# Kernel optimization log

Hardware: AMD Instinct MI355X
Metric: run time of the kernel (lower is better)

## Reference

```python
import jax, jax.numpy as jnp
import numpy as np

N_NODES = 100000
E = 500000
H = 128  # hidden_channels


def setup_inputs() -> dict:
    key = jax.random.key(0)
    ks = jax.random.split(key, 9)
    return {
        "z_pnode": jax.random.normal(ks[0], (N_NODES, H), dtype=jnp.float32),
        "z_onode": jax.random.normal(ks[1], (N_NODES, H), dtype=jnp.float32),
        "ptnp_edge_label_index": jax.random.randint(ks[2], (2, E), 0, N_NODES, dtype=jnp.int64) if jax.config.jax_enable_x64 else jax.random.randint(ks[2], (2, E), 0, N_NODES, dtype=jnp.int32),
        "nptp_edge_label_index": jax.random.randint(ks[3], (2, E), 0, N_NODES, dtype=jnp.int32),
        "nptnp_edge_label_index": jax.random.randint(ks[4], (2, E), 0, N_NODES, dtype=jnp.int32),
        "w1": jax.random.normal(ks[5], (2 * H, H), dtype=jnp.float32) * (1.0 / np.sqrt(2 * H)),
        "b1": jnp.zeros((H,), dtype=jnp.float32),
        "w2": jax.random.normal(ks[6], (H, 1), dtype=jnp.float32) * (1.0 / np.sqrt(H)),
        "b2": jnp.zeros((1,), dtype=jnp.float32),
    }


def reference(z_pnode, z_onode, ptnp_edge_label_index, nptp_edge_label_index,
              nptnp_edge_label_index, w1, b1, w2, b2):
    # Gather endpoint embeddings per edge type and concat along feature dim.
    z_ptnp = jnp.concatenate(
        [z_pnode[ptnp_edge_label_index[0]], z_onode[ptnp_edge_label_index[1]]], axis=-1)
    z_nptp = jnp.concatenate(
        [z_onode[nptp_edge_label_index[0]], z_pnode[nptp_edge_label_index[1]]], axis=-1)
    z_nptnp = jnp.concatenate(
        [z_onode[nptnp_edge_label_index[0]], z_onode[nptnp_edge_label_index[1]]], axis=-1)
    z = jnp.concatenate([z_ptnp, z_nptp, z_nptnp], axis=0)  # [3E, 2H]
    h = jax.nn.relu(z @ w1 + b1)                             # [3E, H]
    out = h @ w2 + b2                                        # [3E, 1]
    return out.reshape(-1)
```

## Files before the change

### kernel.cpp

```cpp
#include <hip/hip_runtime.h>
#include <hip/hip_bf16.h>
#include <stdint.h>

#define H 128
#define NNODES 100000
#define NEDGE 500000
#define MT 32
#define TILES_PER_Z 3125
#define GEMM_GRID 1024

#define BSW_BYTES 65536
#define TBL_ELEMS (NNODES * H)
#define WS_NEEDED ((size_t)BSW_BYTES + 4ULL * TBL_ELEMS * 2ULL)

typedef __bf16 bf16x8 __attribute__((ext_vector_type(8)));
typedef float f32x4 __attribute__((ext_vector_type(4)));

union frag_cast { uint4 u; bf16x8 b; ushort s[8]; };

__device__ __forceinline__ ushort f2bf(float f) {
    __hip_bfloat16 h = __float2bfloat16(f);
    return *(ushort*)&h;
}

__device__ __forceinline__ void bf2_to_f(uint32_t u, float& lo, float& hi) {
    union { uint32_t i; float f; } a, b;
    a.i = u << 16;
    b.i = u & 0xffff0000u;
    lo = a.f;
    hi = b.f;
}

__global__ __launch_bounds__(256) void prep_bsw(const float* __restrict__ w1,
                                                ushort* __restrict__ bsw) {
    int i = blockIdx.x * 256 + threadIdx.x;
    int j = i & 7;
    int n = (i >> 3) & 255;
    int kb = i >> 11;
    int k = kb * 8 + j;
    int r = (n < 128) ? k : (128 + k);
    int c = n & 127;
    bsw[i] = f2bf(w1[r * H + c]);
}

__global__ __launch_bounds__(256, 3) void gemm_tables(
    const float* __restrict__ zp, const float* __restrict__ zo,
    const ushort* __restrict__ bsw, const float* __restrict__ b1,
    ushort* __restrict__ t_ps, ushort* __restrict__ t_pd,
    ushort* __restrict__ t_os, ushort* __restrict__ t_od) {
    __shared__ float abuf[MT * H];

    const int t = threadIdx.x;
    const int wave = t >> 6;
    const int lane = t & 63;
    const int l15 = lane & 15;
    const int quad = lane >> 4;
    const int n0 = wave * 64;
    const int half = wave >> 1;
    const int colbase = n0 - half * 128;

    frag_cast bfr[4][4];
#pragma unroll
    for (int s = 0; s < 4; ++s)
#pragma unroll
        for (int nt = 0; nt < 4; ++nt)
            bfr[s][nt].u = *(const uint4*)(bsw + ((s * 4 + quad) * 256 + n0 + nt * 16 + l15) * 8);

    float bias[4] = {0.f, 0.f, 0.f, 0.f};
    if (half) {
#pragma unroll
        for (int nt = 0; nt < 4; ++nt)
            bias[nt] = b1[colbase + nt * 16 + l15];
    }

    int src_off[4];
    int lds_off[4];
#pragma unroll
    for (int i = 0; i < 4; ++i) {
        const int r = (wave * 4 + i) * 2 + (lane >> 5);
        const int jsrc = (lane & 31) ^ (r & 15);
        src_off[i] = r * H + jsrc * 4;
        lds_off[i] = (wave * 4 + i) * 256;
    }

    for (int tile = blockIdx.x; tile < 2 * TILES_PER_Z; tile += gridDim.x) {
        const int zsel = tile & 1;
        const int node0 = (tile >> 1) * MT;
        const float* __restrict__ ztile =
            (zsel ? zo : zp) + (size_t)node0 * H;

#pragma unroll
        for (int i = 0; i < 4; ++i) {
            const float* gp = ztile + src_off[i];
            float* lp = abuf + lds_off[i];
            __builtin_amdgcn_global_load_lds(
                (const __attribute__((address_space(1))) uint32_t*)gp,
                (__attribute__((address_space(3))) uint32_t*)lp, 16, 0, 0);
        }
        __syncthreads();

        f32x4 acc[2][4];
#pragma unroll
        for (int mt = 0; mt < 2; ++mt)
#pragma unroll
            for (int nt = 0; nt < 4; ++nt)
                acc[mt][nt] = (f32x4){0.f, 0.f, 0.f, 0.f};

#pragma unroll
        for (int s = 0; s < 4; ++s)
#pragma unroll
            for (int mt = 0; mt < 2; ++mt) {
                const int row = mt * 16 + l15;
                const int c = s * 4 + quad;
                const float4 vlo = *(const float4*)(abuf + row * H + ((2 * c) ^ l15) * 4);
                const float4 vhi = *(const float4*)(abuf + row * H + ((2 * c + 1) ^ l15) * 4);
                frag_cast a;
                a.s[0] = f2bf(vlo.x); a.s[1] = f2bf(vlo.y);
                a.s[2] = f2bf(vlo.z); a.s[3] = f2bf(vlo.w);
                a.s[4] = f2bf(vhi.x); a.s[5] = f2bf(vhi.y);
                a.s[6] = f2bf(vhi.z); a.s[7] = f2bf(vhi.w);
#pragma unroll
                for (int nt = 0; nt < 4; ++nt)
                    acc[mt][nt] = __builtin_amdgcn_mfma_f32_16x16x32_bf16(
                        a.b, bfr[s][nt].b, acc[mt][nt], 0, 0, 0);
            }
        __syncthreads();

        ushort* __restrict__ dst =
            zsel ? (half ? t_od : t_os) : (half ? t_pd : t_ps);
#pragma unroll
        for (int mt = 0; mt < 2; ++mt)
#pragma unroll
            for (int nt = 0; nt < 4; ++nt) {
                const int col = colbase + nt * 16 + l15;
#pragma unroll
                for (int r = 0; r < 4; ++r) {
                    const int grow = node0 + mt * 16 + quad * 4 + r;
                    dst[(size_t)grow * H + col] = f2bf(acc[mt][nt][r] + bias[nt]);
                }
            }
    }
}

__global__ __launch_bounds__(256) void edge_kernel(
    const __hip_bfloat16* __restrict__ t_ps, const __hip_bfloat16* __restrict__ t_pd,
    const __hip_bfloat16* __restrict__ t_os, const __hip_bfloat16* __restrict__ t_od,
    const int* __restrict__ ptnp, const int* __restrict__ nptp,
    const int* __restrict__ nptnp,
    const float* __restrict__ w2, const float* __restrict__ b2,
    float* __restrict__ out) {
    const int tid = blockIdx.x * 256 + threadIdx.x;
    const int g = tid >> 4;
    const int lane = tid & 15;

    const __hip_bfloat16 *src_tbl, *dst_tbl;
    int si, di;
    if (g < NEDGE) {
        si = ptnp[g]; di = ptnp[NEDGE + g];
        src_tbl = t_ps; dst_tbl = t_od;
    } else if (g < 2 * NEDGE) {
        const int e = g - NEDGE;
        si = nptp[e]; di = nptp[NEDGE + e];
        src_tbl = t_os; dst_tbl = t_pd;
    } else {
        const int e = g - 2 * NEDGE;
        si = nptnp[e]; di = nptnp[NEDGE + e];
        src_tbl = t_os; dst_tbl = t_od;
    }

    const uint4 s4 = *(const uint4*)(src_tbl + si * H + lane * 8);
    const uint4 d4 = *(const uint4*)(dst_tbl + di * H + lane * 8);
    const float4 w2a = *(const float4*)(w2 + lane * 8);
    const float4 w2b = *(const float4*)(w2 + lane * 8 + 4);

    float s0, s1, d0, d1;
    float sum = 0.f;
    bf2_to_f(s4.x, s0, s1); bf2_to_f(d4.x, d0, d1);
    sum = fmaf(fmaxf(s0 + d0, 0.f), w2a.x, sum);
    sum = fmaf(fmaxf(s1 + d1, 0.f), w2a.y, sum);
    bf2_to_f(s4.y, s0, s1); bf2_to_f(d4.y, d0, d1);
    sum = fmaf(fmaxf(s0 + d0, 0.f), w2a.z, sum);
    sum = fmaf(fmaxf(s1 + d1, 0.f), w2a.w, sum);
    bf2_to_f(s4.z, s0, s1); bf2_to_f(d4.z, d0, d1);
    sum = fmaf(fmaxf(s0 + d0, 0.f), w2b.x, sum);
    sum = fmaf(fmaxf(s1 + d1, 0.f), w2b.y, sum);
    bf2_to_f(s4.w, s0, s1); bf2_to_f(d4.w, d0, d1);
    sum = fmaf(fmaxf(s0 + d0, 0.f), w2b.z, sum);
    sum = fmaf(fmaxf(s1 + d1, 0.f), w2b.w, sum);

    sum += __shfl_down(sum, 8, 16);
    sum += __shfl_down(sum, 4, 16);
    sum += __shfl_down(sum, 2, 16);
    sum += __shfl_down(sum, 1, 16);
    if (lane == 0) out[g] = sum + b2[0];
}

__global__ __launch_bounds__(128) void edge_direct(
    const float* __restrict__ zp, const float* __restrict__ zo,
    const int* __restrict__ ptnp, const int* __restrict__ nptp,
    const int* __restrict__ nptnp,
    const float* __restrict__ w1, const float* __restrict__ b1,
    const float* __restrict__ w2, const float* __restrict__ b2,
    float* __restrict__ out) {
    const int g = blockIdx.x;
    const int j = threadIdx.x;

    const float *src, *dst;
    int si, di;
    if (g < NEDGE) {
        si = ptnp[g]; di = ptnp[NEDGE + g]; src = zp; dst = zo;
    } else if (g < 2 * NEDGE) {
        const int e = g - NEDGE;
        si = nptp[e]; di = nptp[NEDGE + e]; src = zo; dst = zp;
    } else {
        const int e = g - 2 * NEDGE;
        si = nptnp[e]; di = nptnp[NEDGE + e]; src = zo; dst = zo;
    }
    const float* zs = src + si * H;
    const float* zd = dst + di * H;

    float acc = b1[j];
    for (int k = 0; k < H; ++k) acc = fmaf(zs[k], w1[k * H + j], acc);
    for (int k = 0; k < H; ++k) acc = fmaf(zd[k], w1[(H + k) * H + j], acc);
    float v = fmaxf(acc, 0.f) * w2[j];

    for (int off = 32; off > 0; off >>= 1) v += __shfl_down(v, off, 64);
    __shared__ float parts[2];
    if ((j & 63) == 0) parts[j >> 6] = v;
    __syncthreads();
    if (j == 0) out[g] = parts[0] + parts[1] + b2[0];
}

extern "C" void kernel_launch(void* const* d_in, const int* in_sizes, int n_in,
                              void* d_out, int out_size, void* d_ws, size_t ws_size,
                              hipStream_t stream) {
    const float* zp    = (const float*)d_in[0];
    const float* zo    = (const float*)d_in[1];
    const int*   ptnp  = (const int*)d_in[2];
    const int*   nptp  = (const int*)d_in[3];
    const int*   nptnp = (const int*)d_in[4];
    const float* w1    = (const float*)d_in[5];
    const float* b1    = (const float*)d_in[6];
    const float* w2    = (const float*)d_in[7];
    const float* b2    = (const float*)d_in[8];
    float* out = (float*)d_out;

    if (ws_size < WS_NEEDED) {
        edge_direct<<<3 * NEDGE, 128, 0, stream>>>(zp, zo, ptnp, nptp, nptnp,
                                                   w1, b1, w2, b2, out);
        return;
    }

    char* ws = (char*)d_ws;
    ushort* bsw = (ushort*)ws;
    ushort* t_ps = (ushort*)(ws + BSW_BYTES);
    ushort* t_pd = t_ps + TBL_ELEMS;
    ushort* t_os = t_pd + TBL_ELEMS;
    ushort* t_od = t_os + TBL_ELEMS;

    prep_bsw<<<128, 256, 0, stream>>>(w1, bsw);

    gemm_tables<<<GEMM_GRID, 256, 0, stream>>>(
        zp, zo, bsw, b1, t_ps, t_pd, t_os, t_od);

    const int total_threads = 3 * NEDGE * 16;
    edge_kernel<<<total_threads / 256, 256, 0, stream>>>(
        (const __hip_bfloat16*)t_ps, (const __hip_bfloat16*)t_pd,
        (const __hip_bfloat16*)t_os, (const __hip_bfloat16*)t_od,
        ptnp, nptp, nptnp, w2, b2, out);
}
```

Baseline: 270.5 us.

## Double-buffer GEMM input tiles and stage epilogue through LDS for vector stores

The node-table GEMM now prefetches the next tile into a second LDS buffer while the current tile is computed, so global-to-LDS latency overlaps the MFMA work. Results are written to a padded LDS epilogue buffer and then stored to the tables as 16-byte row-contiguous chunks instead of scattered 2-byte stores. The grid shrinks to 768 blocks to suit the larger LDS footprint. The trade is extra LDS use (lower occupancy) and one more pass through shared memory per tile.

```diff
diff --git a/kernel.cpp b/kernel.cpp
--- a/kernel.cpp
+++ b/kernel.cpp
@@ -6,8 +6,9 @@
 #define NNODES 100000
 #define NEDGE 500000
 #define MT 32
-#define TILES_PER_Z 3125
-#define GEMM_GRID 1024
+#define NT2 6250
+#define GEMM_GRID 768
+#define EPI_S 266
 
 #define BSW_BYTES 65536
 #define TBL_ELEMS (NNODES * H)
@@ -48,7 +49,8 @@
     const ushort* __restrict__ bsw, const float* __restrict__ b1,
     ushort* __restrict__ t_ps, ushort* __restrict__ t_pd,
     ushort* __restrict__ t_os, ushort* __restrict__ t_od) {
-    __shared__ float abuf[MT * H];
+    __shared__ float abuf[2][MT * H];
+    __shared__ ushort ebuf[MT * EPI_S];
 
     const int t = threadIdx.x;
     const int wave = t >> 6;
@@ -57,7 +59,6 @@
     const int quad = lane >> 4;
     const int n0 = wave * 64;
     const int half = wave >> 1;
-    const int colbase = n0 - half * 128;
 
     frag_cast bfr[4][4];
 #pragma unroll
@@ -70,11 +71,10 @@
     if (half) {
 #pragma unroll
         for (int nt = 0; nt < 4; ++nt)
-            bias[nt] = b1[colbase + nt * 16 + l15];
-    }
-
-    int src_off[4];
-    int lds_off[4];
+            bias[nt] = b1[(n0 - 128) + nt * 16 + l15];
+    }
+
+    int src_off[4], lds_off[4];
 #pragma unroll
     for (int i = 0; i < 4; ++i) {
         const int r = (wave * 4 + i) * 2 + (lane >> 5);
@@ -83,22 +83,33 @@
         lds_off[i] = (wave * 4 + i) * 256;
     }
 
-    for (int tile = blockIdx.x; tile < 2 * TILES_PER_Z; tile += gridDim.x) {
-        const int zsel = tile & 1;
-        const int node0 = (tile >> 1) * MT;
-        const float* __restrict__ ztile =
-            (zsel ? zo : zp) + (size_t)node0 * H;
-
-#pragma unroll
-        for (int i = 0; i < 4; ++i) {
-            const float* gp = ztile + src_off[i];
-            float* lp = abuf + lds_off[i];
+    int tile = blockIdx.x;
+    if (tile < NT2) {
+        const float* zt = ((tile & 1) ? zo : zp) + (size_t)((tile >> 1) * MT) * H;
+#pragma unroll
+        for (int i = 0; i < 4; ++i)
             __builtin_amdgcn_global_load_lds(
-                (const __attribute__((address_space(1))) uint32_t*)gp,
-                (__attribute__((address_space(3))) uint32_t*)lp, 16, 0, 0);
+                (const __attribute__((address_space(1))) uint32_t*)(zt + src_off[i]),
+                (__attribute__((address_space(3))) uint32_t*)(&abuf[0][0] + lds_off[i]),
+                16, 0, 0);
+    }
+
+    int buf = 0;
+    for (; tile < NT2; tile += GEMM_GRID) {
+        __syncthreads();
+
+        const int nxt = tile + GEMM_GRID;
+        if (nxt < NT2) {
+            const float* zt = ((nxt & 1) ? zo : zp) + (size_t)((nxt >> 1) * MT) * H;
+#pragma unroll
+            for (int i = 0; i < 4; ++i)
+                __builtin_amdgcn_global_load_lds(
+                    (const __attribute__((address_space(1))) uint32_t*)(zt + src_off[i]),
+                    (__attribute__((address_space(3))) uint32_t*)(&abuf[buf ^ 1][0] + lds_off[i]),
+                    16, 0, 0);
         }
-        __syncthreads();
-
+
+        const float* __restrict__ ab = &abuf[buf][0];
         f32x4 acc[2][4];
 #pragma unroll
         for (int mt = 0; mt < 2; ++mt)
@@ -112,8 +123,8 @@
             for (int mt = 0; mt < 2; ++mt) {
                 const int row = mt * 16 + l15;
                 const int c = s * 4 + quad;
-                const float4 vlo = *(const float4*)(abuf + row * H + ((2 * c) ^ l15) * 4);
-                const float4 vhi = *(const float4*)(abuf + row * H + ((2 * c + 1) ^ l15) * 4);
+                const float4 vlo = *(const float4*)(ab + row * H + ((2 * c) ^ l15) * 4);
+                const float4 vhi = *(const float4*)(ab + row * H + ((2 * c + 1) ^ l15) * 4);
                 frag_cast a;
                 a.s[0] = f2bf(vlo.x); a.s[1] = f2bf(vlo.y);
                 a.s[2] = f2bf(vlo.z); a.s[3] = f2bf(vlo.w);
@@ -124,21 +135,36 @@
                     acc[mt][nt] = __builtin_amdgcn_mfma_f32_16x16x32_bf16(
                         a.b, bfr[s][nt].b, acc[mt][nt], 0, 0, 0);
             }
+
+#pragma unroll
+        for (int mt = 0; mt < 2; ++mt)
+#pragma unroll
+            for (int nt = 0; nt < 4; ++nt) {
+                const int col = n0 + nt * 16 + l15;
+#pragma unroll
+                for (int r = 0; r < 4; ++r)
+                    ebuf[(mt * 16 + quad * 4 + r) * EPI_S + col] =
+                        f2bf(acc[mt][nt][r] + bias[nt]);
+            }
+
         __syncthreads();
 
-        ushort* __restrict__ dst =
-            zsel ? (half ? t_od : t_os) : (half ? t_pd : t_ps);
-#pragma unroll
-        for (int mt = 0; mt < 2; ++mt)
-#pragma unroll
-            for (int nt = 0; nt < 4; ++nt) {
-                const int col = colbase + nt * 16 + l15;
-#pragma unroll
-                for (int r = 0; r < 4; ++r) {
-                    const int grow = node0 + mt * 16 + quad * 4 + r;
-                    dst[(size_t)grow * H + col] = f2bf(acc[mt][nt][r] + bias[nt]);
-                }
-            }
+        const int zsel = tile & 1;
+        const int node0 = (tile >> 1) * MT;
+        ushort* __restrict__ stab = zsel ? t_os : t_ps;
+        ushort* __restrict__ dtab = zsel ? t_od : t_pd;
+#pragma unroll
+        for (int i = 0; i < 4; ++i) {
+            const int c = i * 256 + t;
+            const int table = c >> 9;
+            const int row = (c >> 4) & 31;
+            const int ch = c & 15;
+            ushort* __restrict__ dst = table ? dtab : stab;
+            *(uint4*)(dst + (size_t)(node0 + row) * H + ch * 8) =
+                *(const uint4*)(ebuf + row * EPI_S + table * 128 + ch * 8);
+        }
+
+        buf ^= 1;
     }
 }
 
@@ -168,8 +194,8 @@
         src_tbl = t_os; dst_tbl = t_od;
     }
 
-    const uint4 s4 = *(const uint4*)(src_tbl + si * H + lane * 8);
-    const uint4 d4 = *(const uint4*)(dst_tbl + di * H + lane * 8);
+    const uint4 s4 = *(const uint4*)(src_tbl + (size_t)si * H + lane * 8);
+    const uint4 d4 = *(const uint4*)(dst_tbl + (size_t)di * H + lane * 8);
     const float4 w2a = *(const float4*)(w2 + lane * 8);
     const float4 w2b = *(const float4*)(w2 + lane * 8 + 4);
 
```

Result: no change. 266.1 us (-1.6%).
